# Performance work log

Hardware: AMD Instinct MI355X
Metric: run time of the kernel (lower is better)

Reference implementation:

```python
import jax, jax.numpy as jnp
import numpy as np

HIDDEN, NOISE, MLPW, NCOND, DATA, INIT_NOISE = 64, 16, 128, 4, 8, 16
T, B = 128, 8192
TSCALE = 1.0


def _lipswish(x):
    return 0.909 * x * jax.nn.sigmoid(x)


def _mlp(x, Ws, bs):
    for W, b in zip(Ws[:-1], bs[:-1]):
        x = _lipswish(x @ W + b)
    return TSCALE * jnp.tanh(x @ Ws[-1] + bs[-1])  # tanh regularization, tscale=1.0


def setup_inputs():
    key = jax.random.key(0)
    ks = jax.random.split(key, 12)

    def lin(k, fi, fo):
        k1, k2 = jax.random.split(k)
        lim = 1.0 / float(np.sqrt(fi))
        W = jax.random.uniform(k1, (fi, fo), minval=-lim, maxval=lim, dtype=jnp.float32)
        b = jax.random.uniform(k2, (fo,), minval=-lim, maxval=lim, dtype=jnp.float32)
        return W, b

    ind = 1 + HIDDEN + NCOND  # cat([t, x, c0])
    dr_W0, dr_b0 = lin(ks[0], ind, MLPW)
    dr_W1, dr_b1 = lin(ks[1], MLPW, MLPW)
    dr_W2, dr_b2 = lin(ks[2], MLPW, HIDDEN)
    di_W0, di_b0 = lin(ks[3], ind, MLPW)
    di_W1, di_b1 = lin(ks[4], MLPW, MLPW)
    di_W2, di_b2 = lin(ks[5], MLPW, HIDDEN * NOISE)
    init_W, init_b = lin(ks[6], INIT_NOISE + NCOND, HIDDEN)
    ro_W, ro_b = lin(ks[7], HIDDEN + NCOND, DATA)

    ts = jnp.linspace(0.0, 1.0, T, dtype=jnp.float32)
    dt = 1.0 / (T - 1)
    dW = jax.random.normal(ks[8], (T - 1, B, NOISE), dtype=jnp.float32) * float(np.sqrt(dt))
    conditions = jax.random.normal(ks[9], (NCOND,), dtype=jnp.float32)
    return dict(ts=ts, conditions=conditions, dW=dW,
                dr_W0=dr_W0, dr_b0=dr_b0, dr_W1=dr_W1, dr_b1=dr_b1, dr_W2=dr_W2, dr_b2=dr_b2,
                di_W0=di_W0, di_b0=di_b0, di_W1=di_W1, di_b1=di_b1, di_W2=di_W2, di_b2=di_b2,
                init_W=init_W, init_b=init_b, ro_W=ro_W, ro_b=ro_b, batch_size=B)


def reference(ts, conditions, dW, dr_W0, dr_b0, dr_W1, dr_b1, dr_W2, dr_b2,
              di_W0, di_b0, di_W1, di_b1, di_W2, di_b2, init_W, init_b, ro_W, ro_b,
              batch_size):
    drWs, drbs = (dr_W0, dr_W1, dr_W2), (dr_b0, dr_b1, dr_b2)
    diWs, dibs = (di_W0, di_W1, di_W2), (di_b0, di_b1, di_b2)

    h0 = jnp.ones((batch_size, INIT_NOISE), jnp.float32)  # fixed=True initial point
    c0 = jnp.broadcast_to(conditions[None, :], (batch_size, NCOND))
    x0 = jnp.concatenate([h0, c0], 1) @ init_W + init_b  # (B, H)

    def fg(t, x):
        tcol = jnp.full((x.shape[0], 1), t, x.dtype)
        tx = jnp.concatenate([tcol, x, c0], 1)
        f = _mlp(tx, drWs, drbs)  # (B, H)
        g = _mlp(tx, diWs, dibs).reshape(x.shape[0], HIDDEN, NOISE)  # (B, H, M)
        return f, g

    f0, g0 = fg(ts[0], x0)
    dts = jnp.diff(ts)

    def step(carry, inp):
        y, z, fz, gz = carry
        t1, dt, dw = inp
        # reversible Heun (Stratonovich): auxiliary state z, re-used (f,g) at (t_n, z_n)
        z1 = 2.0 * y - z + fz * dt + jnp.einsum('bhm,bm->bh', gz, dw)
        f1, g1 = fg(t1, z1)
        y1 = y + 0.5 * dt * (fz + f1) + 0.5 * jnp.einsum('bhm,bm->bh', gz + g1, dw)
        return (y1, z1, f1, g1), y1

    _, ys = jax.lax.scan(step, (x0, x0, f0, g0), (ts[1:], dts, dW))
    xs = jnp.concatenate([x0[None], ys], 0).transpose(1, 0, 2)  # (B, T, H)
    nT = xs.shape[1]
    cs = jnp.broadcast_to(c0[:, None, :], (batch_size, nT, NCOND))
    out = jnp.concatenate([xs, cs], -1) @ ro_W + ro_b  # (B, T, data)
    ts_e = jnp.broadcast_to(ts[None, :, None], (batch_size, nT, 1))
    # linear_interpolation_coeffs with no NaNs is the identity on the values
    return jnp.concatenate([ts_e, out], -1)  # (B, T, 1 + data)
```

## Files before the change

### kernel.cpp

```cpp
#include <hip/hip_runtime.h>
#include <hip/hip_bf16.h>
#include <cstdint>
#include <cstddef>

#define B_TOT   8192
#define T_TOT   128
#define ROWS    32
#define THREADS 1024

typedef __bf16 bf16x8 __attribute__((ext_vector_type(8)));
typedef float  f32x4  __attribute__((ext_vector_type(4)));

#define WSF_X0    0
#define WSF_BCD   64
#define WSF_BCG   192
#define WSF_ROB   320
#define WSB_SMALL 1536
#define WSB_WD2   (WSB_SMALL + 49152*2)
#define WSB_WG2   (WSB_WD2 + 8192*2)
#define WSB_ROWP  (WSB_WG2 + 131072*2)
#define WSB_TOTAL (WSB_ROWP + 1024*2)

__device__ __forceinline__ unsigned short f2bf(float v){
  union { float f; unsigned u; } x; x.f = v;
  unsigned r = (x.u + 0x7FFFu + ((x.u >> 16) & 1u)) >> 16;
  return (unsigned short)r;
}
__device__ __forceinline__ unsigned cvtpk(float lo, float hi){
  unsigned r;
  asm("v_cvt_pk_bf16_f32 %0, %1, %2" : "=v"(r) : "v"(lo), "v"(hi));
  return r;
}
__device__ __forceinline__ float fexp2(float x){ return __builtin_amdgcn_exp2f(x); }
__device__ __forceinline__ float frcp (float x){ return __builtin_amdgcn_rcpf(x); }
__device__ __forceinline__ float swishf(float x){
  float e = fexp2(-1.44269504088896340f * x);
  return x * frcp(1.0f + e);
}
__device__ __forceinline__ float tanhfast(float x){
  float e = fexp2(2.88539008177792681f * x);
  return 1.0f - 2.0f * frcp(e + 1.0f);
}
__device__ __forceinline__ f32x4 mfma16(bf16x8 a, bf16x8 b, f32x4 c){
  return __builtin_amdgcn_mfma_f32_16x16x32_bf16(a, b, c, 0, 0, 0);
}
__device__ __forceinline__ bf16x8 lds_bfrag(const unsigned short* buf, int rowBytes,
                                            int brow, int kByte){
  int off = brow * rowBytes + kByte;
  off ^= (brow & 7) << 4;
  return *(const bf16x8*)((const char*)buf + off);
}

__global__ void prep_kernel(const float* __restrict__ cond,
    const float* __restrict__ drW0, const float* __restrict__ drb0,
    const float* __restrict__ drW1, const float* __restrict__ drW2,
    const float* __restrict__ diW0, const float* __restrict__ dib0,
    const float* __restrict__ diW1, const float* __restrict__ diW2,
    const float* __restrict__ initW, const float* __restrict__ initb,
    const float* __restrict__ roW,  const float* __restrict__ rob,
    char* __restrict__ ws)
{
  float* wsf = (float*)ws;
  unsigned short* wsm = (unsigned short*)(ws + WSB_SMALL);
  unsigned short* wd2 = (unsigned short*)(ws + WSB_WD2);
  unsigned short* wg2 = (unsigned short*)(ws + WSB_WG2);
  unsigned short* rwp = (unsigned short*)(ws + WSB_ROWP);
  int tid = blockIdx.x * blockDim.x + threadIdx.x;
  int nth = gridDim.x * blockDim.x;

  for (int h = tid; h < 64; h += nth){
    float s = initb[h];
    #pragma unroll
    for (int i = 0; i < 16; i++) s += initW[i*64 + h];
    #pragma unroll
    for (int c = 0; c < 4; c++) s += cond[c] * initW[(16+c)*64 + h];
    wsf[WSF_X0 + h] = s;
  }
  for (int j = tid; j < 128; j += nth){
    float sd = drb0[j], sg = dib0[j];
    #pragma unroll
    for (int c = 0; c < 4; c++){
      sd += cond[c] * drW0[(65+c)*128 + j];
      sg += cond[c] * diW0[(65+c)*128 + j];
    }
    wsf[WSF_BCD + j] = sd; wsf[WSF_BCG + j] = sg;
  }
  for (int d = tid; d < 8; d += nth){
    float s = rob[d];
    #pragma unroll
    for (int c = 0; c < 4; c++) s += cond[c] * roW[(64+c)*8 + d];
    wsf[WSF_ROB + d] = s;
  }
  for (int u = tid; u < 49152; u += nth){
    int j = u & 7, lane = (u >> 3) & 63, frag = u >> 9;
    int k8 = ((lane >> 4) << 3) + j, o16 = lane & 15;
    float v;
    if (frag < 16)      { int kc = frag & 1,      ot = frag >> 1;      v = drW0[(1 + kc*32 + k8)*128 + ot*16 + o16]; }
    else if (frag < 48) { int f = frag - 16; int kc = f & 3, ot = f >> 2; v = 0.909f * drW1[(kc*32 + k8)*128 + ot*16 + o16]; }
    else if (frag < 64) { int f = frag - 48; int kc = f & 1, ot = f >> 1; v = diW0[(1 + kc*32 + k8)*128 + ot*16 + o16]; }
    else                { int f = frag - 64; int kc = f & 3, ot = f >> 2; v = 0.909f * diW1[(kc*32 + k8)*128 + ot*16 + o16]; }
    wsm[u] = f2bf(v);
  }
  for (int u = tid; u < 8192; u += nth){
    int j = u & 7, lane = (u >> 3) & 63, frag = u >> 9, kc = frag & 3, ot = frag >> 2;
    wd2[u] = f2bf(0.909f * drW2[(kc*32 + ((lane>>4)<<3) + j)*64 + ot*16 + (lane & 15)]);
  }
  for (int u = tid; u < 131072; u += nth){
    int j = u & 7, lane = (u >> 3) & 63, frag = u >> 9, kc = frag & 3, ot = frag >> 2;
    wg2[u] = f2bf(0.909f * diW2[(kc*32 + ((lane>>4)<<3) + j)*1024 + ot*16 + (lane & 15)]);
  }
  for (int u = tid; u < 1024; u += nth){
    int j = u & 7, lane = (u >> 3) & 63, kc = u >> 9;
    int k = kc*32 + ((lane>>4)<<3) + j, o = lane & 15;
    rwp[u] = (o < 8) ? f2bf(roW[k*8 + o]) : (unsigned short)0;
  }
}

__global__ __launch_bounds__(THREADS) void sde_kernel(
    const float* __restrict__ dW,  const float* __restrict__ tsg,
    const float* __restrict__ drW0, const float* __restrict__ diW0,
    const float* __restrict__ bd1, const float* __restrict__ bg1,
    const float* __restrict__ bd2, const float* __restrict__ bg2,
    const char* __restrict__ ws, float* __restrict__ out)
{
  __shared__ unsigned short smallW[49152];
  __shared__ unsigned short z1buf[2048];
  __shared__ unsigned short ybuf[2048];
  __shared__ unsigned short h1d[4096];
  __shared__ unsigned short h1g[4096];
  __shared__ unsigned short h2d[4096];
  __shared__ unsigned short h2g[4096];
  __shared__ float f1T[2048];
  __shared__ float tsbuf[128];
  __shared__ float bcdS[128], bcgS[128];
  __shared__ float wtdS[128], wtgS[128];
  __shared__ float bd1S[128], bg1S[128];
  __shared__ float bg2S[1024];
  __shared__ float dwcS[512], dwnS[512];
  __shared__ float robiasS[8];

  const float* wsf = (const float*)ws;
  const unsigned short* wsSmall = (const unsigned short*)(ws + WSB_SMALL);
  const unsigned short* wsWd2   = (const unsigned short*)(ws + WSB_WD2);
  const unsigned short* wsWg2   = (const unsigned short*)(ws + WSB_WG2);
  const unsigned short* wsRoWp  = (const unsigned short*)(ws + WSB_ROWP);

  const int tid = threadIdx.x;
  const int w  = tid >> 6;
  const int l  = tid & 63;
  const int lg = l >> 4;
  const int li = l & 15;
  const int B0 = blockIdx.x * ROWS;
  const int row = tid >> 5;
  const int h0  = (tid & 31) << 1;

  {
    const uint4* src = (const uint4*)wsSmall;
    uint4* dst = (uint4*)smallW;
    for (int i = tid; i < 6144; i += THREADS) dst[i] = src[i];
    for (int i = tid; i < 128; i += THREADS){
      tsbuf[i] = tsg[i];
      bcdS[i] = wsf[WSF_BCD + i]; bcgS[i] = wsf[WSF_BCG + i];
      wtdS[i] = drW0[i];          wtgS[i] = diW0[i];
      bd1S[i] = bd1[i];           bg1S[i] = bg1[i];
    }
    for (int i = tid; i < 1024; i += THREADS) bg2S[i] = bg2[i];
    if (tid < 8) robiasS[tid] = wsf[WSF_ROB + tid];
  }

  float y[2], z[2], fz[2], az[2];
  #pragma unroll
  for (int j = 0; j < 2; j++){ float v = wsf[WSF_X0 + h0 + j]; y[j] = v; z[j] = v; }

  auto writeZ = [&](){
    unsigned v = cvtpk(z[0], z[1]);
    int off = row*128 + (h0 << 1); off ^= (row & 7) << 4;
    *(unsigned*)((char*)z1buf + off) = v;
  };
  auto writeY = [&](){
    unsigned v = cvtpk(y[0], y[1]);
    int off = row*128 + (h0 << 1); off ^= (row & 7) << 4;
    *(unsigned*)((char*)ybuf + off) = v;
  };
  writeZ(); writeY();

  __syncthreads();

  auto OUTPROJ = [&](int tcur){
    const int bm = w - 14, brow = bm*16 + li;
    f32x4 acc = {0.f,0.f,0.f,0.f};
    #pragma unroll
    for (int kc = 0; kc < 2; kc++){
      bf16x8 rw = *(const bf16x8*)(wsRoWp + ((kc*64 + l) << 3));
      bf16x8 yb = lds_bfrag(ybuf, 128, brow, kc*64 + lg*16);
      acc = mfma16(rw, yb, acc);
    }
    float* orow = out + (size_t)(B0 + brow)*1152 + (size_t)tcur*9;
    if (lg < 2){
      #pragma unroll
      for (int r = 0; r < 4; r++) orow[1 + lg*4 + r] = acc[r] + robiasS[lg*4 + r];
    } else if (lg == 2){
      orow[0] = tsbuf[tcur];
    }
  };

  auto PIPE = [&](float tval, int kdwc, int kdwn, int tcur){
    if (tid < 256){
      const float* src = dW + ((tid < 128) ? (size_t)kdwc : (size_t)kdwn)*131072
                            + (size_t)B0*16;
      float* dst = (tid < 128) ? dwcS : dwnS;
      int i = tid & 127;
      *(f32x4*)(dst + i*4) = *(const f32x4*)(src + i*4);
    }
    {
      const int p = w >> 3, ot = w & 7;
      const int base = p ? 24576 : 0;
      unsigned short* hout = p ? h1g : h1d;
      f32x4 acc0 = {0.f,0.f,0.f,0.f}, acc1 = {0.f,0.f,0.f,0.f};
      #pragma unroll
      for (int kc = 0; kc < 2; kc++){
        bf16x8 af = *(const bf16x8*)(smallW + base + ((ot*2 + kc)*64 + l)*8);
        bf16x8 z0 = lds_bfrag(z1buf, 128,      li, kc*64 + lg*16);
        bf16x8 z1 = lds_bfrag(z1buf, 128, 16 + li, kc*64 + lg*16);
        acc0 = mfma16(af, z0, acc0);
        acc1 = mfma16(af, z1, acc1);
      }
      f32x4 bcv = *(const f32x4*)((p ? bcgS : bcdS) + ot*16 + lg*4);
      f32x4 wtv = *(const f32x4*)((p ? wtgS : wtdS) + ot*16 + lg*4);
      #pragma unroll
      for (int bm = 0; bm < 2; bm++){
        const f32x4& acc = bm ? acc1 : acc0;
        int brow = bm*16 + li;
        float xx[4];
        #pragma unroll
        for (int r = 0; r < 4; r++) xx[r] = swishf(acc[r] + bcv[r] + tval*wtv[r]);
        int off = brow*256 + ((ot*16 + lg*4) << 1); off ^= (brow & 7) << 4;
        uint2 v; v.x = cvtpk(xx[0], xx[1]); v.y = cvtpk(xx[2], xx[3]);
        *(uint2*)((char*)hout + off) = v;
      }
      if (tcur >= 0 && w >= 14) OUTPROJ(tcur);
    }
    __syncthreads();
    {
      const int p = w >> 3, ot = w & 7;
      const unsigned short* hin  = p ? h1g : h1d;
      unsigned short*       hout = p ? h2g : h2d;
      const int base = p ? 32768 : 8192;
      f32x4 acc0 = {0.f,0.f,0.f,0.f}, acc1 = {0.f,0.f,0.f,0.f};
      #pragma unroll
      for (int kc = 0; kc < 4; kc++){
        bf16x8 af = *(const bf16x8*)(smallW + base + ((ot*4 + kc)*64 + l)*8);
        bf16x8 hb0 = lds_bfrag(hin, 256,      li, kc*64 + lg*16);
        bf16x8 hb1 = lds_bfrag(hin, 256, 16 + li, kc*64 + lg*16);
        acc0 = mfma16(af, hb0, acc0);
        acc1 = mfma16(af, hb1, acc1);
      }
      f32x4 b1v = *(const f32x4*)((p ? bg1S : bd1S) + ot*16 + lg*4);
      #pragma unroll
      for (int bm = 0; bm < 2; bm++){
        const f32x4& acc = bm ? acc1 : acc0;
        int brow = bm*16 + li;
        float xx[4];
        #pragma unroll
        for (int r = 0; r < 4; r++) xx[r] = swishf(acc[r] + b1v[r]);
        int off = brow*256 + ((ot*16 + lg*4) << 1); off ^= (brow & 7) << 4;
        uint2 v; v.x = cvtpk(xx[0], xx[1]); v.y = cvtpk(xx[2], xx[3]);
        *(uint2*)((char*)hout + off) = v;
      }
    }
    __syncthreads();
    {
      float* bT = (float*)h1d;
      float* aT = (float*)h1g;
      if (w < 8){
        const int ot = w >> 1, bm = w & 1, brow = bm*16 + li;
        f32x4 acc = {0.f,0.f,0.f,0.f};
        #pragma unroll
        for (int kc = 0; kc < 4; kc++){
          bf16x8 wf = *(const bf16x8*)(wsWd2 + ((ot*4 + kc)*64 + l)*8);
          bf16x8 db = lds_bfrag(h2d, 256, brow, kc*64 + lg*16);
          acc = mfma16(wf, db, acc);
        }
        f32x4 bdv = *(const f32x4*)(bd2 + ot*16 + lg*4);
        #pragma unroll
        for (int r = 0; r < 4; r++){
          int h = ot*16 + lg*4 + r;
          f1T[h*32 + (brow ^ (h & 31))] = tanhfast(acc[r] + bdv[r]);
        }
      }
      #pragma unroll 1
      for (int ot = 0; ot < 4; ot++){
        const int h = w*4 + ot;
        f32x4 acc0 = {0.f,0.f,0.f,0.f}, acc1 = {0.f,0.f,0.f,0.f};
        #pragma unroll
        for (int kc = 0; kc < 4; kc++){
          bf16x8 fk = *(const bf16x8*)(wsWg2 + (((h*4 + kc)*64 + l) << 3));
          bf16x8 g0 = lds_bfrag(h2g, 256,      li, kc*64 + lg*16);
          bf16x8 g1 = lds_bfrag(h2g, 256, 16 + li, kc*64 + lg*16);
          acc0 = mfma16(fk, g0, acc0);
          acc1 = mfma16(fk, g1, acc1);
        }
        f32x4 bgv = *(const f32x4*)(bg2S + h*16 + lg*4);
        #pragma unroll
        for (int bm = 0; bm < 2; bm++){
          const f32x4& acc = bm ? acc1 : acc0;
          const int brow = bm*16 + li;
          f32x4 dwcv = *(const f32x4*)(dwcS + brow*16 + lg*4);
          f32x4 dwnv = *(const f32x4*)(dwnS + brow*16 + lg*4);
          float bs = 0.f, as_ = 0.f;
          #pragma unroll
          for (int r = 0; r < 4; r++){
            float g = tanhfast(acc[r] + bgv[r]);
            bs  += g * dwcv[r];
            as_ += g * dwnv[r];
          }
          bs  += __shfl_xor(bs, 16);  bs  += __shfl_xor(bs, 32);
          as_ += __shfl_xor(as_, 16); as_ += __shfl_xor(as_, 32);
          const int idx = h*32 + (brow ^ (h & 31));
          if (lg == 0)      bT[idx] = bs;
          else if (lg == 1) aT[idx] = as_;
        }
      }
    }
  };

  PIPE(tsbuf[0], 0, 0, -1);
  __syncthreads();
  {
    #pragma unroll
    for (int j = 0; j < 2; j++){
      int h = h0 + j; int idx = h*32 + (row ^ (h & 31));
      fz[j] = f1T[idx];
      az[j] = ((const float*)h1g)[idx];
    }
    float dt0 = tsbuf[1] - tsbuf[0];
    #pragma unroll
    for (int j = 0; j < 2; j++) z[j] = 2.f*y[j] - z[j] + fz[j]*dt0 + az[j];
    writeZ();
  }
  __syncthreads();

  for (int k = 0; k < 127; k++){
    PIPE(tsbuf[k+1], k, (k < 126) ? (k+1) : 126, k);
    __syncthreads();
    float f1[2], bb[2], an[2];
    #pragma unroll
    for (int j = 0; j < 2; j++){
      int h = h0 + j; int idx = h*32 + (row ^ (h & 31));
      f1[j] = f1T[idx];
      bb[j] = ((const float*)h1d)[idx];
      an[j] = ((const float*)h1g)[idx];
    }
    float dtk = tsbuf[k+1] - tsbuf[k];
    #pragma unroll
    for (int j = 0; j < 2; j++){
      y[j] += 0.5f*dtk*(fz[j] + f1[j]) + 0.5f*(az[j] + bb[j]);
      fz[j] = f1[j]; az[j] = an[j];
    }
    writeY();
    if (k < 126){
      float dtn = tsbuf[k+2] - tsbuf[k+1];
      #pragma unroll
      for (int j = 0; j < 2; j++) z[j] = 2.f*y[j] - z[j] + fz[j]*dtn + az[j];
      writeZ();
    }
    __syncthreads();
  }

  if (w >= 14) OUTPROJ(127);
}

extern "C" void kernel_launch(void* const* d_in, const int* in_sizes, int n_in,
                              void* d_out, int out_size, void* d_ws, size_t ws_size,
                              hipStream_t stream)
{
  const float* ts   = (const float*)d_in[0];
  const float* cond = (const float*)d_in[1];
  const float* dW   = (const float*)d_in[2];
  const float* drW0 = (const float*)d_in[3];
  const float* drb0 = (const float*)d_in[4];
  const float* drW1 = (const float*)d_in[5];
  const float* drb1 = (const float*)d_in[6];
  const float* drW2 = (const float*)d_in[7];
  const float* drb2 = (const float*)d_in[8];
  const float* diW0 = (const float*)d_in[9];
  const float* dib0 = (const float*)d_in[10];
  const float* diW1 = (const float*)d_in[11];
  const float* dib1 = (const float*)d_in[12];
  const float* diW2 = (const float*)d_in[13];
  const float* dib2 = (const float*)d_in[14];
  const float* initW= (const float*)d_in[15];
  const float* initb= (const float*)d_in[16];
  const float* roW  = (const float*)d_in[17];
  const float* rob  = (const float*)d_in[18];
  char* ws = (char*)d_ws;
  if (ws_size < (size_t)WSB_TOTAL) return;

  prep_kernel<<<dim3(256), dim3(256), 0, stream>>>(
      cond, drW0, drb0, drW1, drW2, diW0, dib0, diW1, diW2,
      initW, initb, roW, rob, ws);
  sde_kernel<<<dim3(256), dim3(THREADS), 0, stream>>>(
      dW, ts, drW0, diW0, drb1, dib1, drb2, dib2, ws, (float*)d_out);
}
```

Baseline: 1.008 ms.

## Re-layout LDS activation buffers into k-chunked swizzle and hoist B-fragment loads

Changes the LDS layout of the z/y/hidden activation buffers to a k-chunk-major swizzled format so that MFMA B-fragments are read with precomputed per-thread offsets, and pads the dW staging buffers to cut bank conflicts. In the diffusion output layer the h2g fragments are loaded once into registers and reused across all four output tiles, and that loop is now fully unrolled. The drift output layer moves to warps 8-15 and the readout projection to warps 0-1 in the third stage, which balances work across the two halves of the block. In exchange, register pressure rises from holding eight bf16x8 fragments plus the precomputed offsets.

After: 1.024 ms. No clear change (+1.6%).

```diff
diff --git a/kernel.cpp b/kernel.cpp
--- a/kernel.cpp
+++ b/kernel.cpp
@@ -43,12 +43,6 @@
 }
 __device__ __forceinline__ f32x4 mfma16(bf16x8 a, bf16x8 b, f32x4 c){
   return __builtin_amdgcn_mfma_f32_16x16x32_bf16(a, b, c, 0, 0, 0);
-}
-__device__ __forceinline__ bf16x8 lds_bfrag(const unsigned short* buf, int rowBytes,
-                                            int brow, int kByte){
-  int off = brow * rowBytes + kByte;
-  off ^= (brow & 7) << 4;
-  return *(const bf16x8*)((const char*)buf + off);
 }
 
 __global__ void prep_kernel(const float* __restrict__ cond,
@@ -135,8 +129,9 @@
   __shared__ float bcdS[128], bcgS[128];
   __shared__ float wtdS[128], wtgS[128];
   __shared__ float bd1S[128], bg1S[128];
+  __shared__ float bd2S[64];
   __shared__ float bg2S[1024];
-  __shared__ float dwcS[512], dwnS[512];
+  __shared__ float dwcS[640], dwnS[640];
   __shared__ float robiasS[8];
 
   const float* wsf = (const float*)ws;
@@ -150,9 +145,24 @@
   const int l  = tid & 63;
   const int lg = l >> 4;
   const int li = l & 15;
+  const int p  = w >> 3;
+  const int ot = w & 7;
   const int B0 = blockIdx.x * ROWS;
   const int row = tid >> 5;
   const int h0  = (tid & 31) << 1;
+
+  const int aEven = lg*512 + ((li ^ lg) << 4);
+  const int aOdd  = aEven ^ 64;
+  const int gW    = (ot*2 + (lg>>1)) & 7;
+  const int wOff  = (ot*2 + (lg>>1))*512 + ((li ^ gW) << 4) + ((lg & 1) << 3);
+  const int gZ    = h0 >> 3;
+  const int zOff  = gZ*512 + ((row ^ (gZ & 7)) << 4) + ((h0 & 7) << 1);
+  const int dOff  = li*80 + lg*16;
+  const int sOff1 = (p ? 49152 : 0)     + ot*2048 + l*16;
+  const int sOff2 = (p ? 65536 : 16384) + ot*4096 + l*16;
+  const int upd0  = h0*32 + (row ^ (h0 & 31));
+  const int upd1  = (h0+1)*32 + (row ^ ((h0+1) & 31));
+  const int otD   = (w - 8) >> 1, bmD = (w - 8) & 1;
 
   {
     const uint4* src = (const uint4*)wsSmall;
@@ -165,6 +175,7 @@
       bd1S[i] = bd1[i];           bg1S[i] = bg1[i];
     }
     for (int i = tid; i < 1024; i += THREADS) bg2S[i] = bg2[i];
+    if (tid < 64) bd2S[tid] = bd2[tid];
     if (tid < 8) robiasS[tid] = wsf[WSF_ROB + tid];
   }
 
@@ -172,29 +183,25 @@
   #pragma unroll
   for (int j = 0; j < 2; j++){ float v = wsf[WSF_X0 + h0 + j]; y[j] = v; z[j] = v; }
 
-  auto writeZ = [&](){
-    unsigned v = cvtpk(z[0], z[1]);
-    int off = row*128 + (h0 << 1); off ^= (row & 7) << 4;
-    *(unsigned*)((char*)z1buf + off) = v;
+  auto writeZ = [&](){ *(unsigned*)((char*)z1buf + zOff) = cvtpk(z[0], z[1]); };
+  auto writeY = [&](){ *(unsigned*)((char*)ybuf  + zOff) = cvtpk(y[0], y[1]); };
+  writeZ(); writeY();
+
+  __syncthreads();
+
+  auto rdfrag = [&](const unsigned short* buf, int kc, int bm) -> bf16x8 {
+    int off = ((kc & 1) ? aOdd : aEven) + kc*2048 + bm*256;
+    return *(const bf16x8*)((const char*)buf + off);
   };
-  auto writeY = [&](){
-    unsigned v = cvtpk(y[0], y[1]);
-    int off = row*128 + (h0 << 1); off ^= (row & 7) << 4;
-    *(unsigned*)((char*)ybuf + off) = v;
-  };
-  writeZ(); writeY();
-
-  __syncthreads();
 
   auto OUTPROJ = [&](int tcur){
-    const int bm = w - 14, brow = bm*16 + li;
     f32x4 acc = {0.f,0.f,0.f,0.f};
     #pragma unroll
     for (int kc = 0; kc < 2; kc++){
-      bf16x8 rw = *(const bf16x8*)(wsRoWp + ((kc*64 + l) << 3));
-      bf16x8 yb = lds_bfrag(ybuf, 128, brow, kc*64 + lg*16);
-      acc = mfma16(rw, yb, acc);
-    }
+      bf16x8 rw = *(const bf16x8*)((const char*)wsRoWp + kc*1024 + l*16);
+      acc = mfma16(rw, rdfrag(ybuf, kc, w), acc);
+    }
+    const int brow = w*16 + li;
     float* orow = out + (size_t)(B0 + brow)*1152 + (size_t)tcur*9;
     if (lg < 2){
       #pragma unroll
@@ -210,103 +217,94 @@
                             + (size_t)B0*16;
       float* dst = (tid < 128) ? dwcS : dwnS;
       int i = tid & 127;
-      *(f32x4*)(dst + i*4) = *(const f32x4*)(src + i*4);
+      *(f32x4*)(dst + (i>>2)*20 + (i&3)*4) = *(const f32x4*)(src + i*4);
     }
     {
-      const int p = w >> 3, ot = w & 7;
-      const int base = p ? 24576 : 0;
-      unsigned short* hout = p ? h1g : h1d;
       f32x4 acc0 = {0.f,0.f,0.f,0.f}, acc1 = {0.f,0.f,0.f,0.f};
       #pragma unroll
       for (int kc = 0; kc < 2; kc++){
-        bf16x8 af = *(const bf16x8*)(smallW + base + ((ot*2 + kc)*64 + l)*8);
-        bf16x8 z0 = lds_bfrag(z1buf, 128,      li, kc*64 + lg*16);
-        bf16x8 z1 = lds_bfrag(z1buf, 128, 16 + li, kc*64 + lg*16);
-        acc0 = mfma16(af, z0, acc0);
-        acc1 = mfma16(af, z1, acc1);
+        bf16x8 af = *(const bf16x8*)((const char*)smallW + sOff1 + kc*1024);
+        acc0 = mfma16(af, rdfrag(z1buf, kc, 0), acc0);
+        acc1 = mfma16(af, rdfrag(z1buf, kc, 1), acc1);
       }
       f32x4 bcv = *(const f32x4*)((p ? bcgS : bcdS) + ot*16 + lg*4);
       f32x4 wtv = *(const f32x4*)((p ? wtgS : wtdS) + ot*16 + lg*4);
+      unsigned short* hout = p ? h1g : h1d;
       #pragma unroll
       for (int bm = 0; bm < 2; bm++){
         const f32x4& acc = bm ? acc1 : acc0;
-        int brow = bm*16 + li;
         float xx[4];
         #pragma unroll
         for (int r = 0; r < 4; r++) xx[r] = swishf(acc[r] + bcv[r] + tval*wtv[r]);
-        int off = brow*256 + ((ot*16 + lg*4) << 1); off ^= (brow & 7) << 4;
         uint2 v; v.x = cvtpk(xx[0], xx[1]); v.y = cvtpk(xx[2], xx[3]);
-        *(uint2*)((char*)hout + off) = v;
-      }
-      if (tcur >= 0 && w >= 14) OUTPROJ(tcur);
+        *(uint2*)((char*)hout + wOff + bm*256) = v;
+      }
     }
     __syncthreads();
     {
-      const int p = w >> 3, ot = w & 7;
       const unsigned short* hin  = p ? h1g : h1d;
       unsigned short*       hout = p ? h2g : h2d;
-      const int base = p ? 32768 : 8192;
       f32x4 acc0 = {0.f,0.f,0.f,0.f}, acc1 = {0.f,0.f,0.f,0.f};
       #pragma unroll
       for (int kc = 0; kc < 4; kc++){
-        bf16x8 af = *(const bf16x8*)(smallW + base + ((ot*4 + kc)*64 + l)*8);
-        bf16x8 hb0 = lds_bfrag(hin, 256,      li, kc*64 + lg*16);
-        bf16x8 hb1 = lds_bfrag(hin, 256, 16 + li, kc*64 + lg*16);
-        acc0 = mfma16(af, hb0, acc0);
-        acc1 = mfma16(af, hb1, acc1);
+        bf16x8 af = *(const bf16x8*)((const char*)smallW + sOff2 + kc*1024);
+        acc0 = mfma16(af, rdfrag(hin, kc, 0), acc0);
+        acc1 = mfma16(af, rdfrag(hin, kc, 1), acc1);
       }
       f32x4 b1v = *(const f32x4*)((p ? bg1S : bd1S) + ot*16 + lg*4);
       #pragma unroll
       for (int bm = 0; bm < 2; bm++){
         const f32x4& acc = bm ? acc1 : acc0;
-        int brow = bm*16 + li;
         float xx[4];
         #pragma unroll
         for (int r = 0; r < 4; r++) xx[r] = swishf(acc[r] + b1v[r]);
-        int off = brow*256 + ((ot*16 + lg*4) << 1); off ^= (brow & 7) << 4;
         uint2 v; v.x = cvtpk(xx[0], xx[1]); v.y = cvtpk(xx[2], xx[3]);
-        *(uint2*)((char*)hout + off) = v;
+        *(uint2*)((char*)hout + wOff + bm*256) = v;
       }
     }
     __syncthreads();
     {
       float* bT = (float*)h1d;
       float* aT = (float*)h1g;
-      if (w < 8){
-        const int ot = w >> 1, bm = w & 1, brow = bm*16 + li;
+      bf16x8 gf[2][4];
+      #pragma unroll
+      for (int kc = 0; kc < 4; kc++){
+        gf[0][kc] = rdfrag(h2g, kc, 0);
+        gf[1][kc] = rdfrag(h2g, kc, 1);
+      }
+      if (w >= 8){
         f32x4 acc = {0.f,0.f,0.f,0.f};
         #pragma unroll
         for (int kc = 0; kc < 4; kc++){
-          bf16x8 wf = *(const bf16x8*)(wsWd2 + ((ot*4 + kc)*64 + l)*8);
-          bf16x8 db = lds_bfrag(h2d, 256, brow, kc*64 + lg*16);
-          acc = mfma16(wf, db, acc);
+          bf16x8 wf = *(const bf16x8*)((const char*)wsWd2 + otD*4096 + kc*1024 + l*16);
+          acc = mfma16(wf, rdfrag(h2d, kc, bmD), acc);
         }
-        f32x4 bdv = *(const f32x4*)(bd2 + ot*16 + lg*4);
+        f32x4 bdv = *(const f32x4*)(bd2S + otD*16 + lg*4);
+        const int browD = bmD*16 + li;
         #pragma unroll
         for (int r = 0; r < 4; r++){
-          int h = ot*16 + lg*4 + r;
-          f1T[h*32 + (brow ^ (h & 31))] = tanhfast(acc[r] + bdv[r]);
+          int h = otD*16 + lg*4 + r;
+          f1T[h*32 + (browD ^ (h & 31))] = tanhfast(acc[r] + bdv[r]);
         }
-      }
-      #pragma unroll 1
-      for (int ot = 0; ot < 4; ot++){
-        const int h = w*4 + ot;
+      } else if (tcur >= 0 && w < 2){
+        OUTPROJ(tcur);
+      }
+      #pragma unroll
+      for (int o = 0; o < 4; o++){
+        const int h = w*4 + o;
         f32x4 acc0 = {0.f,0.f,0.f,0.f}, acc1 = {0.f,0.f,0.f,0.f};
         #pragma unroll
         for (int kc = 0; kc < 4; kc++){
-          bf16x8 fk = *(const bf16x8*)(wsWg2 + (((h*4 + kc)*64 + l) << 3));
-          bf16x8 g0 = lds_bfrag(h2g, 256,      li, kc*64 + lg*16);
-          bf16x8 g1 = lds_bfrag(h2g, 256, 16 + li, kc*64 + lg*16);
-          acc0 = mfma16(fk, g0, acc0);
-          acc1 = mfma16(fk, g1, acc1);
+          bf16x8 fk = *(const bf16x8*)((const char*)wsWg2 + (size_t)((h*4 + kc)*1024) + l*16);
+          acc0 = mfma16(fk, gf[0][kc], acc0);
+          acc1 = mfma16(fk, gf[1][kc], acc1);
         }
         f32x4 bgv = *(const f32x4*)(bg2S + h*16 + lg*4);
         #pragma unroll
         for (int bm = 0; bm < 2; bm++){
           const f32x4& acc = bm ? acc1 : acc0;
-          const int brow = bm*16 + li;
-          f32x4 dwcv = *(const f32x4*)(dwcS + brow*16 + lg*4);
-          f32x4 dwnv = *(const f32x4*)(dwnS + brow*16 + lg*4);
+          f32x4 dwcv = *(const f32x4*)((const char*)dwcS + dOff + bm*1280);
+          f32x4 dwnv = *(const f32x4*)((const char*)dwnS + dOff + bm*1280);
           float bs = 0.f, as_ = 0.f;
           #pragma unroll
           for (int r = 0; r < 4; r++){
@@ -316,6 +314,7 @@
           }
           bs  += __shfl_xor(bs, 16);  bs  += __shfl_xor(bs, 32);
           as_ += __shfl_xor(as_, 16); as_ += __shfl_xor(as_, 32);
+          const int brow = bm*16 + li;
           const int idx = h*32 + (brow ^ (h & 31));
           if (lg == 0)      bT[idx] = bs;
           else if (lg == 1) aT[idx] = as_;
@@ -329,7 +328,7 @@
   {
     #pragma unroll
     for (int j = 0; j < 2; j++){
-      int h = h0 + j; int idx = h*32 + (row ^ (h & 31));
+      int idx = j ? upd1 : upd0;
       fz[j] = f1T[idx];
       az[j] = ((const float*)h1g)[idx];
     }
@@ -346,7 +345,7 @@
     float f1[2], bb[2], an[2];
     #pragma unroll
     for (int j = 0; j < 2; j++){
-      int h = h0 + j; int idx = h*32 + (row ^ (h & 31));
+      int idx = j ? upd1 : upd0;
       f1[j] = f1T[idx];
       bb[j] = ((const float*)h1d)[idx];
       an[j] = ((const float*)h1g)[idx];
@@ -367,7 +366,7 @@
     __syncthreads();
   }
 
-  if (w >= 14) OUTPROJ(127);
+  if (w < 2) OUTPROJ(127);
 }
 
 extern "C" void kernel_launch(void* const* d_in, const int* in_sizes, int n_in,
```
